# Kernel tuning notes

Measured on AMD Instinct MI355X. Metric: run time of the kernel, lower is better.

The kernel has to match this reference:

```python
import jax, jax.numpy as jnp
import numpy as np

E, H, I = 8, 2048, 4096      # experts, hidden, intermediate
T, K = 1024, 2               # tokens, top_k
GS = 128                     # quantization group size


def setup_inputs() -> dict:
    key = jax.random.key(0)
    ks = jax.random.split(key, 9)
    x = jax.random.normal(ks[0], (T, H), dtype=jnp.float32)
    # packed int4: two nibbles per uint8, [out_features, in_features // 2]
    gu_packed = jax.random.randint(ks[1], (E, 2 * I, H // 2), 0, 256, dtype=jnp.int32).astype(jnp.uint8)
    dn_packed = jax.random.randint(ks[2], (E, H, I // 2), 0, 256, dtype=jnp.int32).astype(jnp.uint8)
    # small positive scales; zeros chosen so dequantized values center near 0
    gu_scales = jax.random.uniform(ks[3], (E, 2 * I, H // GS), dtype=jnp.float32) * 0.02 + 0.001
    gu_zeros = -7.5 * gu_scales + 0.001 * jax.random.normal(ks[4], gu_scales.shape, dtype=jnp.float32)
    dn_scales = jax.random.uniform(ks[5], (E, H, I // GS), dtype=jnp.float32) * 0.02 + 0.001
    dn_zeros = -7.5 * dn_scales + 0.001 * jax.random.normal(ks[6], dn_scales.shape, dtype=jnp.float32)
    router_indices = jax.random.randint(ks[7], (T, K), 0, E, dtype=jnp.int32)
    rw = jax.random.uniform(ks[8], (T, K), dtype=jnp.float32) + 0.1
    routing_weights = rw / jnp.sum(rw, axis=-1, keepdims=True)
    return {
        "x": x,
        "gu_packed": gu_packed, "gu_scales": gu_scales, "gu_zeros": gu_zeros,
        "dn_packed": dn_packed, "dn_scales": dn_scales, "dn_zeros": dn_zeros,
        "router_indices": router_indices, "routing_weights": routing_weights,
        "group_size": GS,
    }


def _dequantize_packed_weight(packed, scales, zeros, in_features, group_size):
    """Unpack uint8 nibbles (high at even cols, low at odd cols), apply
    per-group scale and zero-point: w = q * scale + zero."""
    out_f = packed.shape[0]
    high = (packed >> 4) & 15
    low = packed & 15
    # interleave: column 0::2 = high nibble, 1::2 = low nibble
    unpacked = jnp.stack([high, low], axis=-1).reshape(out_f, -1).astype(scales.dtype)
    n_groups = scales.shape[1]
    grouped = unpacked.reshape(out_f, n_groups, group_size)
    dq = grouped * scales[:, :, None] + zeros[:, :, None]
    return dq.reshape(out_f, n_groups * group_size)[:, :in_features]


def reference(x, gu_packed, gu_scales, gu_zeros, dn_packed, dn_scales, dn_zeros,
              router_indices, routing_weights, group_size):
    num_experts = gu_packed.shape[0]
    hidden = x.shape[-1]
    inter = dn_packed.shape[2] * 2
    # per-token per-expert combine coefficient [T, E]
    one_hot = jax.nn.one_hot(router_indices, num_experts, dtype=x.dtype)  # [T, K, E]
    coef = jnp.einsum("tke,tk->te", one_hot, routing_weights)
    out = jnp.zeros_like(x)
    for e in range(num_experts):
        gu_w = _dequantize_packed_weight(gu_packed[e], gu_scales[e], gu_zeros[e], hidden, group_size)  # [2I, H]
        dn_w = _dequantize_packed_weight(dn_packed[e], dn_scales[e], dn_zeros[e], inter, group_size)   # [H, I]
        gu = x @ gu_w.T                     # [T, 2I]
        gate, up = jnp.split(gu, 2, axis=-1)
        h = jax.nn.gelu(gate, approximate=True) * up  # [T, I]
        out = out + coef[:, e:e + 1] * (h @ dn_w.T)   # [T, H]
    return out
```

## Files before the change

### kernel.cpp

```cpp
#include <hip/hip_runtime.h>
#include <hip/hip_bf16.h>
#include <stdint.h>

#define E_ 8
#define H_ 2048
#define I_ 4096
#define T_ 1024
#define K_ 2
#define GS_ 128
#define NPAIR (T_ * K_)

#define BM 128
#define BN 64
#define BK 64

#define CH(r, c) ((((c) ^ ((r) & 7)) << 3))

typedef __attribute__((ext_vector_type(8))) short s16x8;
typedef __attribute__((ext_vector_type(4))) float f32x4;

static __device__ __forceinline__ unsigned short f2bf(float f) {
    __hip_bfloat16 h = __float2bfloat16(f);
    return __builtin_bit_cast(unsigned short, h);
}
static __device__ __forceinline__ uint32_t pk2(float lo16, float hi16) {
    uint32_t a = __builtin_bit_cast(uint32_t, lo16) + 0x8000u;
    uint32_t b = __builtin_bit_cast(uint32_t, hi16) + 0x8000u;
    return (a >> 16) | (b & 0xffff0000u);
}

__global__ void x2bf_kernel(const float* __restrict__ x, unsigned short* __restrict__ xb) {
    int i = (blockIdx.x * 256 + threadIdx.x) * 8;
    float4 a = *(const float4*)(x + i);
    float4 b = *(const float4*)(x + i + 4);
    unsigned short t[8];
    t[0] = f2bf(a.x); t[1] = f2bf(a.y); t[2] = f2bf(a.z); t[3] = f2bf(a.w);
    t[4] = f2bf(b.x); t[5] = f2bf(b.y); t[6] = f2bf(b.z); t[7] = f2bf(b.w);
    *(s16x8*)(xb + i) = *(s16x8*)t;
}

__global__ void zero_f4(float4* p, int n4) {
    int i = blockIdx.x * blockDim.x + threadIdx.x;
    if (i < n4) p[i] = make_float4(0.f, 0.f, 0.f, 0.f);
}

__global__ void router_kernel(const int* __restrict__ ridx,
                              const float* __restrict__ rw,
                              int* __restrict__ seg,
                              int* __restrict__ ptok,
                              float* __restrict__ pw)
{
    __shared__ int cnt[E_];
    __shared__ int cur[E_];
    int tid = threadIdx.x;
    if (tid < E_) cnt[tid] = 0;
    __syncthreads();
    for (int p = tid; p < NPAIR; p += blockDim.x)
        atomicAdd(&cnt[ridx[p]], 1);
    __syncthreads();
    if (tid == 0) {
        int s = 0;
        for (int e = 0; e < E_; e++) { seg[e] = s; cur[e] = s; s += cnt[e]; }
        seg[E_] = s;
    }
    __syncthreads();
    for (int p = tid; p < NPAIR; p += blockDim.x) {
        int e = ridx[p];
        int pos = atomicAdd(&cur[e], 1);
        ptok[pos] = p >> 1;
        pw[pos] = rw[p];
    }
}

static __device__ __forceinline__ void dq_chunk(int4 q, float sc, float zp,
                                                unsigned short* dst) {
    uint32_t r[4];
    int qa[4] = {q.x, q.y, q.z, q.w};
#pragma unroll
    for (int j = 0; j < 4; j++) {
        uint32_t byte = (uint32_t)qa[j] & 0xffu;
        float fh = (float)(byte >> 4) * sc + zp;
        float fl = (float)(byte & 15u) * sc + zp;
        r[j] = pk2(fh, fl);
    }
    *(uint4*)dst = make_uint4(r[0], r[1], r[2], r[3]);
}

__global__ __launch_bounds__(256, 3) void gemm1_kernel(
    const unsigned short* __restrict__ xb,
    const int* __restrict__ gu_packed,
    const float* __restrict__ gu_scales,
    const float* __restrict__ gu_zeros,
    const int* __restrict__ seg,
    const int* __restrict__ ptok,
    unsigned short* __restrict__ h_act)
{
    const int e = blockIdx.z;
    const int seg0 = seg[e], seg1 = seg[e + 1];
    const int m0 = blockIdx.y * BM;
    if (seg0 + m0 >= seg1) return;
    const int n0 = blockIdx.x * BN;

    __shared__ __align__(16) unsigned short sX[BM * 64];
    __shared__ __align__(16) unsigned short sG[BN * 64];
    __shared__ __align__(16) unsigned short sU[BN * 64];

    const int tid = threadIdx.x;
    const int lane = tid & 63;
    const int wave = tid >> 6;
    const int wm = (wave >> 1) * 64;
    const int wn = (wave & 1) * 32;
    const int quad = lane >> 4;
    const int l16 = lane & 15;

    const int xr = tid >> 1;
    const int xc0 = (tid & 1) * 4;
    int slotX = seg0 + m0 + xr;
    if (slotX > NPAIR - 1) slotX = NPAIR - 1;
    const unsigned short* xrow = xb + (size_t)ptok[slotX] * H_ + xc0 * 8;

    const int wr = tid >> 2;
    const int wc0 = (tid & 3) * 2;
    const int ng = n0 + wr;
    const int nu = n0 + I_ + wr;
    const int* gprow = gu_packed + ((size_t)e * (2 * I_) + ng) * (H_ / 2) + (tid & 3) * 8;
    const int* uprow = gu_packed + ((size_t)e * (2 * I_) + nu) * (H_ / 2) + (tid & 3) * 8;
    const float* gsrow = gu_scales + ((size_t)e * (2 * I_) + ng) * (H_ / GS_);
    const float* gzrow = gu_zeros  + ((size_t)e * (2 * I_) + ng) * (H_ / GS_);
    const float* usrow = gu_scales + ((size_t)e * (2 * I_) + nu) * (H_ / GS_);
    const float* uzrow = gu_zeros  + ((size_t)e * (2 * I_) + nu) * (H_ / GS_);

    f32x4 accg[4][2], accu[4][2];
#pragma unroll
    for (int mi = 0; mi < 4; mi++)
#pragma unroll
        for (int ni = 0; ni < 2; ni++) {
            accg[mi][ni] = (f32x4){0.f, 0.f, 0.f, 0.f};
            accu[mi][ni] = (f32x4){0.f, 0.f, 0.f, 0.f};
        }

    s16x8 rX[4];
    int4 rG[2], rU[2];
    float rgs, rgz, rus, ruz;

    {
        const s16x8* xp = (const s16x8*)(xrow);
        rX[0] = xp[0]; rX[1] = xp[1]; rX[2] = xp[2]; rX[3] = xp[3];
        const int4* gp = (const int4*)(gprow);
        rG[0] = gp[0]; rG[1] = gp[1];
        const int4* up = (const int4*)(uprow);
        rU[0] = up[0]; rU[1] = up[1];
        rgs = gsrow[0]; rgz = gzrow[0]; rus = usrow[0]; ruz = uzrow[0];
    }

    for (int k0 = 0; k0 < H_; k0 += BK) {
        *(s16x8*)&sX[(xr << 6) + CH(xr, xc0 + 0)] = rX[0];
        *(s16x8*)&sX[(xr << 6) + CH(xr, xc0 + 1)] = rX[1];
        *(s16x8*)&sX[(xr << 6) + CH(xr, xc0 + 2)] = rX[2];
        *(s16x8*)&sX[(xr << 6) + CH(xr, xc0 + 3)] = rX[3];
        dq_chunk(rG[0], rgs, rgz, &sG[(wr << 6) + CH(wr, wc0)]);
        dq_chunk(rG[1], rgs, rgz, &sG[(wr << 6) + CH(wr, wc0 + 1)]);
        dq_chunk(rU[0], rus, ruz, &sU[(wr << 6) + CH(wr, wc0)]);
        dq_chunk(rU[1], rus, ruz, &sU[(wr << 6) + CH(wr, wc0 + 1)]);
        __syncthreads();

        if (k0 + BK < H_) {
            const int k1 = k0 + BK;
            const s16x8* xp = (const s16x8*)(xrow + k1);
            rX[0] = xp[0]; rX[1] = xp[1]; rX[2] = xp[2]; rX[3] = xp[3];
            const int4* gp = (const int4*)(gprow + (k1 >> 1));
            rG[0] = gp[0]; rG[1] = gp[1];
            const int4* up = (const int4*)(uprow + (k1 >> 1));
            rU[0] = up[0]; rU[1] = up[1];
            const int g = k1 >> 7;
            rgs = gsrow[g]; rgz = gzrow[g]; rus = usrow[g]; ruz = uzrow[g];
        }

#pragma unroll
        for (int ks = 0; ks < 2; ks++) {
            const int cb = ks * 4 + quad;
            s16x8 af[4], gf[2], uf[2];
#pragma unroll
            for (int i = 0; i < 4; i++) {
                const int r = wm + i * 16 + l16;
                af[i] = *(const s16x8*)&sX[(r << 6) + CH(r, cb)];
            }
#pragma unroll
            for (int i = 0; i < 2; i++) {
                const int r = wn + i * 16 + l16;
                gf[i] = *(const s16x8*)&sG[(r << 6) + CH(r, cb)];
                uf[i] = *(const s16x8*)&sU[(r << 6) + CH(r, cb)];
            }
#pragma unroll
            for (int mi = 0; mi < 4; mi++)
#pragma unroll
                for (int ni = 0; ni < 2; ni++) {
                    accg[mi][ni] = __builtin_amdgcn_mfma_f32_16x16x32_bf16(af[mi], gf[ni], accg[mi][ni], 0, 0, 0);
                    accu[mi][ni] = __builtin_amdgcn_mfma_f32_16x16x32_bf16(af[mi], uf[ni], accu[mi][ni], 0, 0, 0);
                }
        }
        __syncthreads();
    }

#pragma unroll
    for (int mi = 0; mi < 4; mi++) {
#pragma unroll
        for (int rr = 0; rr < 4; rr++) {
            const int row = wm + mi * 16 + quad * 4 + rr;
            const int slot = seg0 + m0 + row;
            if (slot < seg1) {
#pragma unroll
                for (int ni = 0; ni < 2; ni++) {
                    const int col = n0 + wn + ni * 16 + l16;
                    float gv = accg[mi][ni][rr];
                    float uv = accu[mi][ni][rr];
                    float t = tanhf(0.7978845608028654f * (gv + 0.044715f * gv * gv * gv));
                    float hv = 0.5f * gv * (1.0f + t) * uv;
                    h_act[(size_t)slot * I_ + col] = f2bf(hv);
                }
            }
        }
    }
}

__global__ __launch_bounds__(256, 3) void gemm2_kernel(
    const unsigned short* __restrict__ h_act,
    const int* __restrict__ dn_packed,
    const float* __restrict__ dn_scales,
    const float* __restrict__ dn_zeros,
    const int* __restrict__ seg,
    const int* __restrict__ ptok,
    const float* __restrict__ pw,
    float* __restrict__ out)
{
    const int e = blockIdx.z;
    const int seg0 = seg[e], seg1 = seg[e + 1];
    const int m0 = blockIdx.y * BM;
    if (seg0 + m0 >= seg1) return;
    const int n0 = blockIdx.x * BN;

    __shared__ __align__(16) unsigned short sA[BM * 64];
    __shared__ __align__(16) unsigned short sW[BN * 64];

    const int tid = threadIdx.x;
    const int lane = tid & 63;
    const int wave = tid >> 6;
    const int wm = (wave >> 1) * 64;
    const int wn = (wave & 1) * 32;
    const int quad = lane >> 4;
    const int l16 = lane & 15;

    const int ar = tid >> 1;
    const int ac0 = (tid & 1) * 4;
    int slotA = seg0 + m0 + ar;
    if (slotA > NPAIR - 1) slotA = NPAIR - 1;
    const unsigned short* arow = h_act + (size_t)slotA * I_ + ac0 * 8;

    const int wr = tid >> 2;
    const int wc0 = (tid & 3) * 2;
    const int nw = n0 + wr;
    const int* wprow = dn_packed + ((size_t)e * H_ + nw) * (I_ / 2) + (tid & 3) * 8;
    const float* wsrow = dn_scales + ((size_t)e * H_ + nw) * (I_ / GS_);
    const float* wzrow = dn_zeros  + ((size_t)e * H_ + nw) * (I_ / GS_);

    f32x4 acc[4][2];
#pragma unroll
    for (int mi = 0; mi < 4; mi++)
#pragma unroll
        for (int ni = 0; ni < 2; ni++)
            acc[mi][ni] = (f32x4){0.f, 0.f, 0.f, 0.f};

    s16x8 rA[4];
    int4 rW[2];
    float rs, rz;

    {
        const s16x8* ap = (const s16x8*)(arow);
        rA[0] = ap[0]; rA[1] = ap[1]; rA[2] = ap[2]; rA[3] = ap[3];
        const int4* wp = (const int4*)(wprow);
        rW[0] = wp[0]; rW[1] = wp[1];
        rs = wsrow[0]; rz = wzrow[0];
    }

    for (int k0 = 0; k0 < I_; k0 += BK) {
        *(s16x8*)&sA[(ar << 6) + CH(ar, ac0 + 0)] = rA[0];
        *(s16x8*)&sA[(ar << 6) + CH(ar, ac0 + 1)] = rA[1];
        *(s16x8*)&sA[(ar << 6) + CH(ar, ac0 + 2)] = rA[2];
        *(s16x8*)&sA[(ar << 6) + CH(ar, ac0 + 3)] = rA[3];
        dq_chunk(rW[0], rs, rz, &sW[(wr << 6) + CH(wr, wc0)]);
        dq_chunk(rW[1], rs, rz, &sW[(wr << 6) + CH(wr, wc0 + 1)]);
        __syncthreads();

        if (k0 + BK < I_) {
            const int k1 = k0 + BK;
            const s16x8* ap = (const s16x8*)(arow + k1);
            rA[0] = ap[0]; rA[1] = ap[1]; rA[2] = ap[2]; rA[3] = ap[3];
            const int4* wp = (const int4*)(wprow + (k1 >> 1));
            rW[0] = wp[0]; rW[1] = wp[1];
            const int g = k1 >> 7;
            rs = wsrow[g]; rz = wzrow[g];
        }

#pragma unroll
        for (int ks = 0; ks < 2; ks++) {
            const int cb = ks * 4 + quad;
            s16x8 af[4], wf[2];
#pragma unroll
            for (int i = 0; i < 4; i++) {
                const int r = wm + i * 16 + l16;
                af[i] = *(const s16x8*)&sA[(r << 6) + CH(r, cb)];
            }
#pragma unroll
            for (int i = 0; i < 2; i++) {
                const int r = wn + i * 16 + l16;
                wf[i] = *(const s16x8*)&sW[(r << 6) + CH(r, cb)];
            }
#pragma unroll
            for (int mi = 0; mi < 4; mi++)
#pragma unroll
                for (int ni = 0; ni < 2; ni++)
                    acc[mi][ni] = __builtin_amdgcn_mfma_f32_16x16x32_bf16(af[mi], wf[ni], acc[mi][ni], 0, 0, 0);
        }
        __syncthreads();
    }

#pragma unroll
    for (int mi = 0; mi < 4; mi++) {
#pragma unroll
        for (int rr = 0; rr < 4; rr++) {
            const int row = wm + mi * 16 + quad * 4 + rr;
            const int slot = seg0 + m0 + row;
            if (slot < seg1) {
                const int tok = ptok[slot];
                const float cf = pw[slot];
#pragma unroll
                for (int ni = 0; ni < 2; ni++) {
                    const int col = n0 + wn + ni * 16 + l16;
                    atomicAdd(&out[(size_t)tok * H_ + col], cf * acc[mi][ni][rr]);
                }
            }
        }
    }
}

extern "C" void kernel_launch(void* const* d_in, const int* in_sizes, int n_in,
                              void* d_out, int out_size, void* d_ws, size_t ws_size,
                              hipStream_t stream) {
    const float* x    = (const float*)d_in[0];
    const int*   gu_p = (const int*)d_in[1];
    const float* gu_s = (const float*)d_in[2];
    const float* gu_z = (const float*)d_in[3];
    const int*   dn_p = (const int*)d_in[4];
    const float* dn_s = (const float*)d_in[5];
    const float* dn_z = (const float*)d_in[6];
    const int*   ridx = (const int*)d_in[7];
    const float* rw   = (const float*)d_in[8];

    char* ws = (char*)d_ws;
    int*            seg   = (int*)ws;
    int*            ptok  = (int*)(ws + 256);
    float*          pw    = (float*)(ws + 256 + NPAIR * 4);
    unsigned short* h_act = (unsigned short*)(ws + 32768);
    unsigned short* xb    = (unsigned short*)(ws + 32768 + (size_t)NPAIR * I_ * 2);

    float* out = (float*)d_out;

    x2bf_kernel<<<T_ * H_ / (256 * 8), 256, 0, stream>>>(x, xb);
    zero_f4<<<(T_ * H_ / 4 + 255) / 256, 256, 0, stream>>>((float4*)out, T_ * H_ / 4);
    router_kernel<<<1, 256, 0, stream>>>(ridx, rw, seg, ptok, pw);
    gemm1_kernel<<<dim3(I_ / BN, NPAIR / BM, E_), 256, 0, stream>>>(
        xb, gu_p, gu_s, gu_z, seg, ptok, h_act);
    gemm2_kernel<<<dim3(H_ / BN, NPAIR / BM, E_), 256, 0, stream>>>(
        h_act, dn_p, dn_s, dn_z, seg, ptok, pw, out);
}
```

Baseline: 690.2 us.

## Switch GEMMs to fp16 with magic-number packed int4 dequant

Switches activations, dequantized weights and MFMA instructions from bf16 to fp16. The int4 dequant now uses the 0x6400 magic-bias trick with packed half2 fused multiply-add instead of per-nibble float converts and manual bf16 rounding. The goal is fewer VALU instructions in the dequant stage, which runs inside the main loop. Launch bounds also go from 3 to 5 waves per SIMD to push occupancy. Risks: fp16 range and precision for scales, zero-points and GELU outputs, and register spilling under the tighter bound.

```diff
diff --git a/kernel.cpp b/kernel.cpp
--- a/kernel.cpp
+++ b/kernel.cpp
@@ -1,5 +1,4 @@
 #include <hip/hip_runtime.h>
-#include <hip/hip_bf16.h>
 #include <stdint.h>
 
 #define E_ 8
@@ -17,26 +16,25 @@
 #define CH(r, c) ((((c) ^ ((r) & 7)) << 3))
 
 typedef __attribute__((ext_vector_type(8))) short s16x8;
+typedef _Float16 f16x2 __attribute__((ext_vector_type(2)));
+typedef _Float16 f16x8 __attribute__((ext_vector_type(8)));
 typedef __attribute__((ext_vector_type(4))) float f32x4;
 
-static __device__ __forceinline__ unsigned short f2bf(float f) {
-    __hip_bfloat16 h = __float2bfloat16(f);
+static __device__ __forceinline__ unsigned short f2h(float f) {
+    _Float16 h = (_Float16)f;
     return __builtin_bit_cast(unsigned short, h);
 }
-static __device__ __forceinline__ uint32_t pk2(float lo16, float hi16) {
-    uint32_t a = __builtin_bit_cast(uint32_t, lo16) + 0x8000u;
-    uint32_t b = __builtin_bit_cast(uint32_t, hi16) + 0x8000u;
-    return (a >> 16) | (b & 0xffff0000u);
-}
-
-__global__ void x2bf_kernel(const float* __restrict__ x, unsigned short* __restrict__ xb) {
+static __device__ __forceinline__ uint32_t pkrtz(float lo, float hi) {
+    return __builtin_bit_cast(uint32_t, __builtin_amdgcn_cvt_pkrtz(lo, hi));
+}
+
+__global__ void x2h_kernel(const float* __restrict__ x, unsigned short* __restrict__ xh) {
     int i = (blockIdx.x * 256 + threadIdx.x) * 8;
     float4 a = *(const float4*)(x + i);
     float4 b = *(const float4*)(x + i + 4);
-    unsigned short t[8];
-    t[0] = f2bf(a.x); t[1] = f2bf(a.y); t[2] = f2bf(a.z); t[3] = f2bf(a.w);
-    t[4] = f2bf(b.x); t[5] = f2bf(b.y); t[6] = f2bf(b.z); t[7] = f2bf(b.w);
-    *(s16x8*)(xb + i) = *(s16x8*)t;
+    uint4 st = make_uint4(pkrtz(a.x, a.y), pkrtz(a.z, a.w),
+                          pkrtz(b.x, b.y), pkrtz(b.z, b.w));
+    *(uint4*)(xh + i) = st;
 }
 
 __global__ void zero_f4(float4* p, int n4) {
@@ -72,22 +70,24 @@
     }
 }
 
-static __device__ __forceinline__ void dq_chunk(int4 q, float sc, float zp,
+static __device__ __forceinline__ void dq_chunk(int4 q, f16x2 sc, f16x2 zp,
                                                 unsigned short* dst) {
     uint32_t r[4];
     int qa[4] = {q.x, q.y, q.z, q.w};
+    const f16x2 k1024 = {(_Float16)1024.f, (_Float16)1024.f};
 #pragma unroll
     for (int j = 0; j < 4; j++) {
-        uint32_t byte = (uint32_t)qa[j] & 0xffu;
-        float fh = (float)(byte >> 4) * sc + zp;
-        float fl = (float)(byte & 15u) * sc + zp;
-        r[j] = pk2(fh, fl);
+        uint32_t b = (uint32_t)qa[j];
+        uint32_t p = 0x64006400u | (b >> 4) | ((b & 0xfu) << 16);
+        f16x2 ph = __builtin_bit_cast(f16x2, p);
+        f16x2 w = (ph - k1024) * sc + zp;
+        r[j] = __builtin_bit_cast(uint32_t, w);
     }
     *(uint4*)dst = make_uint4(r[0], r[1], r[2], r[3]);
 }
 
-__global__ __launch_bounds__(256, 3) void gemm1_kernel(
-    const unsigned short* __restrict__ xb,
+__global__ __launch_bounds__(256, 5) void gemm1_kernel(
+    const unsigned short* __restrict__ xh,
     const int* __restrict__ gu_packed,
     const float* __restrict__ gu_scales,
     const float* __restrict__ gu_zeros,
@@ -117,7 +117,7 @@
     const int xc0 = (tid & 1) * 4;
     int slotX = seg0 + m0 + xr;
     if (slotX > NPAIR - 1) slotX = NPAIR - 1;
-    const unsigned short* xrow = xb + (size_t)ptok[slotX] * H_ + xc0 * 8;
+    const unsigned short* xrow = xh + (size_t)ptok[slotX] * H_ + xc0 * 8;
 
     const int wr = tid >> 2;
     const int wc0 = (tid & 3) * 2;
@@ -158,10 +158,16 @@
         *(s16x8*)&sX[(xr << 6) + CH(xr, xc0 + 1)] = rX[1];
         *(s16x8*)&sX[(xr << 6) + CH(xr, xc0 + 2)] = rX[2];
         *(s16x8*)&sX[(xr << 6) + CH(xr, xc0 + 3)] = rX[3];
-        dq_chunk(rG[0], rgs, rgz, &sG[(wr << 6) + CH(wr, wc0)]);
-        dq_chunk(rG[1], rgs, rgz, &sG[(wr << 6) + CH(wr, wc0 + 1)]);
-        dq_chunk(rU[0], rus, ruz, &sU[(wr << 6) + CH(wr, wc0)]);
-        dq_chunk(rU[1], rus, ruz, &sU[(wr << 6) + CH(wr, wc0 + 1)]);
+        {
+            f16x2 gs2 = {(_Float16)rgs, (_Float16)rgs};
+            f16x2 gz2 = {(_Float16)rgz, (_Float16)rgz};
+            f16x2 us2 = {(_Float16)rus, (_Float16)rus};
+            f16x2 uz2 = {(_Float16)ruz, (_Float16)ruz};
+            dq_chunk(rG[0], gs2, gz2, &sG[(wr << 6) + CH(wr, wc0)]);
+            dq_chunk(rG[1], gs2, gz2, &sG[(wr << 6) + CH(wr, wc0 + 1)]);
+            dq_chunk(rU[0], us2, uz2, &sU[(wr << 6) + CH(wr, wc0)]);
+            dq_chunk(rU[1], us2, uz2, &sU[(wr << 6) + CH(wr, wc0 + 1)]);
+        }
         __syncthreads();
 
         if (k0 + BK < H_) {
@@ -179,24 +185,24 @@
 #pragma unroll
         for (int ks = 0; ks < 2; ks++) {
             const int cb = ks * 4 + quad;
-            s16x8 af[4], gf[2], uf[2];
+            f16x8 af[4], gf[2], uf[2];
 #pragma unroll
             for (int i = 0; i < 4; i++) {
                 const int r = wm + i * 16 + l16;
-                af[i] = *(const s16x8*)&sX[(r << 6) + CH(r, cb)];
+                af[i] = *(const f16x8*)&sX[(r << 6) + CH(r, cb)];
             }
 #pragma unroll
             for (int i = 0; i < 2; i++) {
                 const int r = wn + i * 16 + l16;
-                gf[i] = *(const s16x8*)&sG[(r << 6) + CH(r, cb)];
-                uf[i] = *(const s16x8*)&sU[(r << 6) + CH(r, cb)];
+                gf[i] = *(const f16x8*)&sG[(r << 6) + CH(r, cb)];
+                uf[i] = *(const f16x8*)&sU[(r << 6) + CH(r, cb)];
             }
 #pragma unroll
             for (int mi = 0; mi < 4; mi++)
 #pragma unroll
                 for (int ni = 0; ni < 2; ni++) {
-                    accg[mi][ni] = __builtin_amdgcn_mfma_f32_16x16x32_bf16(af[mi], gf[ni], accg[mi][ni], 0, 0, 0);
-                    accu[mi][ni] = __builtin_amdgcn_mfma_f32_16x16x32_bf16(af[mi], uf[ni], accu[mi][ni], 0, 0, 0);
+                    accg[mi][ni] = __builtin_amdgcn_mfma_f32_16x16x32_f16(af[mi], gf[ni], accg[mi][ni], 0, 0, 0);
+                    accu[mi][ni] = __builtin_amdgcn_mfma_f32_16x16x32_f16(af[mi], uf[ni], accu[mi][ni], 0, 0, 0);
                 }
         }
         __syncthreads();
@@ -216,14 +222,14 @@
                     float uv = accu[mi][ni][rr];
                     float t = tanhf(0.7978845608028654f * (gv + 0.044715f * gv * gv * gv));
                     float hv = 0.5f * gv * (1.0f + t) * uv;
-                    h_act[(size_t)slot * I_ + col] = f2bf(hv);
+                    h_act[(size_t)slot * I_ + col] = f2h(hv);
                 }
             }
         }
     }
 }
 
-__global__ __launch_bounds__(256, 3) void gemm2_kernel(
+__global__ __launch_bounds__(256, 5) void gemm2_kernel(
     const unsigned short* __restrict__ h_act,
     const int* __restrict__ dn_packed,
     const float* __restrict__ dn_scales,
@@ -287,8 +293,12 @@
         *(s16x8*)&sA[(ar << 6) + CH(ar, ac0 + 1)] = rA[1];
         *(s16x8*)&sA[(ar << 6) + CH(ar, ac0 + 2)] = rA[2];
         *(s16x8*)&sA[(ar << 6) + CH(ar, ac0 + 3)] = rA[3];
-        dq_chunk(rW[0], rs, rz, &sW[(wr << 6) + CH(wr, wc0)]);
-        dq_chunk(rW[1], rs, rz, &sW[(wr << 6) + CH(wr, wc0 + 1)]);
+        {
+            f16x2 ws2 = {(_Float16)rs, (_Float16)rs};
+            f16x2 wz2 = {(_Float16)rz, (_Float16)rz};
+            dq_chunk(rW[0], ws2, wz2, &sW[(wr << 6) + CH(wr, wc0)]);
+            dq_chunk(rW[1], ws2, wz2, &sW[(wr << 6) + CH(wr, wc0 + 1)]);
+        }
         __syncthreads();
 
         if (k0 + BK < I_) {
@@ -304,22 +314,22 @@
 #pragma unroll
         for (int ks = 0; ks < 2; ks++) {
             const int cb = ks * 4 + quad;
-            s16x8 af[4], wf[2];
+            f16x8 af[4], wf[2];
 #pragma unroll
             for (int i = 0; i < 4; i++) {
                 const int r = wm + i * 16 + l16;
-                af[i] = *(const s16x8*)&sA[(r << 6) + CH(r, cb)];
+                af[i] = *(const f16x8*)&sA[(r << 6) + CH(r, cb)];
             }
 #pragma unroll
             for (int i = 0; i < 2; i++) {
                 const int r = wn + i * 16 + l16;
-                wf[i] = *(const s16x8*)&sW[(r << 6) + CH(r, cb)];
+                wf[i] = *(const f16x8*)&sW[(r << 6) + CH(r, cb)];
             }
 #pragma unroll
             for (int mi = 0; mi < 4; mi++)
 #pragma unroll
                 for (int ni = 0; ni < 2; ni++)
-                    acc[mi][ni] = __builtin_amdgcn_mfma_f32_16x16x32_bf16(af[mi], wf[ni], acc[mi][ni], 0, 0, 0);
+                    acc[mi][ni] = __builtin_amdgcn_mfma_f32_16x16x32_f16(af[mi], wf[ni], acc[mi][ni], 0, 0, 0);
         }
         __syncthreads();
     }
@@ -361,15 +371,15 @@
     int*            ptok  = (int*)(ws + 256);
     float*          pw    = (float*)(ws + 256 + NPAIR * 4);
     unsigned short* h_act = (unsigned short*)(ws + 32768);
-    unsigned short* xb    = (unsigned short*)(ws + 32768 + (size_t)NPAIR * I_ * 2);
+    unsigned short* xh    = (unsigned short*)(ws + 32768 + (size_t)NPAIR * I_ * 2);
 
     float* out = (float*)d_out;
 
-    x2bf_kernel<<<T_ * H_ / (256 * 8), 256, 0, stream>>>(x, xb);
+    x2h_kernel<<<T_ * H_ / (256 * 8), 256, 0, stream>>>(x, xh);
     zero_f4<<<(T_ * H_ / 4 + 255) / 256, 256, 0, stream>>>((float4*)out, T_ * H_ / 4);
     router_kernel<<<1, 256, 0, stream>>>(ridx, rw, seg, ptok, pw);
     gemm1_kernel<<<dim3(I_ / BN, NPAIR / BM, E_), 256, 0, stream>>>(
-        xb, gu_p, gu_s, gu_z, seg, ptok, h_act);
+        xh, gu_p, gu_s, gu_z, seg, ptok, h_act);
     gemm2_kernel<<<dim3(H_ / BN, NPAIR / BM, E_), 256, 0, stream>>>(
         h_act, dn_p, dn_s, dn_z, seg, ptok, pw, out);
 }
```

Result: slower. 1.618 ms (+134.5%).
